# Optimization experiments

Hardware: AMD Instinct MI355X
Metric: run time of the kernel (lower is better)

The kernel has to match this reference:

```python
import jax, jax.numpy as jnp
import numpy as np

VOCAB, D, H = 100000, 128, 256
B, T = 64, 512


def setup_inputs() -> dict:
    key = jax.random.key(0)
    ks = jax.random.split(key, 7)
    path = jax.random.randint(ks[0], (B, T), 0, VOCAB, dtype=jnp.int32)
    valid_len = jax.random.randint(ks[1], (B,), 1, T + 1, dtype=jnp.int32)
    embedding = jax.random.normal(ks[2], (VOCAB, D), dtype=jnp.float32)
    s_ih = 1.0 / np.sqrt(H)
    W_ih = jax.random.uniform(ks[3], (4 * H, D), jnp.float32, -s_ih, s_ih)
    W_hh = jax.random.uniform(ks[4], (4 * H, H), jnp.float32, -s_ih, s_ih)
    b_ih = jax.random.uniform(ks[5], (4 * H,), jnp.float32, -s_ih, s_ih)
    b_hh = jax.random.uniform(ks[6], (4 * H,), jnp.float32, -s_ih, s_ih)
    return {"path": path, "valid_len": valid_len, "embedding": embedding,
            "W_ih": W_ih, "W_hh": W_hh, "b_ih": b_ih, "b_hh": b_hh}


def _lstm_last(x, valid_len, W_ih, W_hh, b_ih, b_hh):
    # x: [B, T, D] -> last-valid hidden state [B, H]
    Bx, Tx, _ = x.shape
    Hd = W_hh.shape[1]
    # precompute input projections for all steps: [T, B, 4H]
    xp = jnp.einsum('btd,gd->tbg', x, W_ih) + b_ih + b_hh

    def step(carry, xg):
        h, c = carry
        gates = xg + h @ W_hh.T  # [B, 4H]
        i, f, g, o = jnp.split(gates, 4, axis=-1)  # pytorch gate order i,f,g,o
        c = jax.nn.sigmoid(f) * c + jax.nn.sigmoid(i) * jnp.tanh(g)
        h = jax.nn.sigmoid(o) * jnp.tanh(c)
        return (h, c), h

    h0 = jnp.zeros((Bx, Hd), x.dtype)
    c0 = jnp.zeros((Bx, Hd), x.dtype)
    _, hs = jax.lax.scan(step, (h0, c0), xp)  # hs: [T, B, H]
    # gather output at t = valid_len - 1 (packed LSTM never advances past valid_len)
    return hs[valid_len - 1, jnp.arange(Bx)]


def reference(path, valid_len, embedding, W_ih, W_hh, b_ih, b_hh):
    x = embedding[path]  # [B, T, D] irregular gather
    return _lstm_last(x, valid_len, W_ih, W_hh, b_ih, b_hh)
```

## Files before the change

kernel.cpp:

```cpp
#include <hip/hip_runtime.h>
#include <stdint.h>


#define BB 64
#define TT 512
#define DD 128
#define HH 256

typedef __fp16 half2v __attribute__((ext_vector_type(2)));

__device__ __forceinline__ uint32_t pk_f16(float lo, float hi) {
    half2v h = __builtin_amdgcn_cvt_pkrtz(lo, hi);
    return __builtin_bit_cast(uint32_t, h);
}

__device__ __forceinline__ float dot2(uint32_t a, uint32_t b, float acc) {
#if __has_builtin(__builtin_amdgcn_fdot2)
    return __builtin_amdgcn_fdot2(__builtin_bit_cast(half2v, a),
                                  __builtin_bit_cast(half2v, b), acc, false);
#else
    half2v av = __builtin_bit_cast(half2v, a);
    half2v bv = __builtin_bit_cast(half2v, b);
    acc += (float)av[0] * (float)bv[0];
    acc += (float)av[1] * (float)bv[1];
    return acc;
#endif
}

__device__ __forceinline__ float fsig(float x)  { return 1.f / (1.f + __expf(-x)); }
__device__ __forceinline__ float ftanh(float x) { return 1.f - 2.f / (__expf(2.f * x) + 1.f); }

__global__ __launch_bounds__(1024, 4)
void lstm_cluster_kernel(const int* __restrict__ path, const int* __restrict__ vlen,
                         const float* __restrict__ emb, const float* __restrict__ Wih,
                         const float* __restrict__ Whh, const float* __restrict__ bih,
                         const float* __restrict__ bhh, float* __restrict__ out,
                         float* hslot ) {
    const int b   = blockIdx.x & (BB - 1);
    const int k   = blockIdx.x >> 6;
    const int tid = threadIdx.x;
    const int r   = tid >> 2;
    const int q   = tid & 3;
    const int g   = r >> 6;
    const int u   = r & 63;
    const int grow = (g << 8) + (k << 6) + u;

    __shared__ uint32_t h_pk[4][40];
    __shared__ uint32_t x_pk[2][4][24];
    __shared__ float    G[256];
    __shared__ int      path_l[TT];

    uint32_t whh[32];
    {
        const float* wr = Whh + grow * HH + (q << 6);
#pragma unroll
        for (int c = 0; c < 32; ++c) whh[c] = pk_f16(wr[2 * c], wr[2 * c + 1]);
    }
    uint32_t wih[16];
    {
        const float* wr = Wih + grow * DD + (q << 5);
#pragma unroll
        for (int c = 0; c < 16; ++c) wih[c] = pk_f16(wr[2 * c], wr[2 * c + 1]);
    }
    const float bias = bih[grow] + bhh[grow];
    const int   L    = vlen[b];

    if (tid < TT)  path_l[tid] = path[b * TT + tid];
    if (tid < 160) ((uint32_t*)h_pk)[tid] = 0u;
    __syncthreads();

    float xr_next = 0.f;
    if (tid < DD) {
        float x0 = emb[(size_t)path_l[0] * DD + tid];
        float hi = __shfl_xor(x0, 1);
        if (!(tid & 1)) x_pk[0][tid >> 5][(tid & 31) >> 1] = pk_f16(x0, hi);
        xr_next = emb[(size_t)path_l[L > 1 ? 1 : 0] * DD + tid];
    }
    float c_state = 0.f;
    __syncthreads();

    for (int t = 0; t < L; ++t) {
        const int slot  = t & 1;
        const int phase = (t >> 1) & 1;

        float xr_pf = 0.f;
        if (tid < DD) {
            int tpf = (t + 2 < TT) ? t + 2 : TT - 1;
            xr_pf = emb[(size_t)path_l[tpf] * DD + tid];
        }

        float acc = 0.f;
#pragma unroll
        for (int c = 0; c < 8; ++c) {
            uint4 hv = *(const uint4*)&h_pk[q][c << 2];
            acc = dot2(whh[(c << 2) + 0], hv.x, acc);
            acc = dot2(whh[(c << 2) + 1], hv.y, acc);
            acc = dot2(whh[(c << 2) + 2], hv.z, acc);
            acc = dot2(whh[(c << 2) + 3], hv.w, acc);
        }
#pragma unroll
        for (int c = 0; c < 4; ++c) {
            uint4 xv = *(const uint4*)&x_pk[slot][q][c << 2];
            acc = dot2(wih[(c << 2) + 0], xv.x, acc);
            acc = dot2(wih[(c << 2) + 1], xv.y, acc);
            acc = dot2(wih[(c << 2) + 2], xv.z, acc);
            acc = dot2(wih[(c << 2) + 3], xv.w, acc);
        }

        acc += __shfl_xor(acc, 1);
        acc += __shfl_xor(acc, 2);
        if (q == 0) G[r] = acc + bias;
        __syncthreads();

        if (tid < DD) {
            float hi = __shfl_xor(xr_next, 1);
            if (!(tid & 1)) x_pk[slot ^ 1][tid >> 5][(tid & 31) >> 1] = pk_f16(xr_next, hi);
        }
        if (tid < 64) {
            float gi = fsig(G[tid]);
            float gf = fsig(G[64 + tid]);
            float gg = ftanh(G[128 + tid]);
            float go = fsig(G[192 + tid]);
            c_state  = gf * c_state + gi * gg;
            float h  = go * ftanh(c_state);
            if (t == L - 1) out[b * HH + (k << 6) + tid] = h;
            __hip_atomic_store(&hslot[(slot * BB + b) * HH + (k << 6) + tid],
                               phase ? h + 8.f : h,
                               __ATOMIC_RELAXED, __HIP_MEMORY_SCOPE_AGENT);
        }
        xr_next = xr_pf;

        if (t < L - 1) {
            if (tid < HH) {
                float* addr = &hslot[(slot * BB + b) * HH + tid];
                float v;
                int spins = 0;
                if (phase == 0) {
                    do { v = __hip_atomic_load(addr, __ATOMIC_RELAXED, __HIP_MEMORY_SCOPE_AGENT);
                    } while (!(v > -4.f && v < 4.f) && ++spins < 200000);
                } else {
                    do { v = __hip_atomic_load(addr, __ATOMIC_RELAXED, __HIP_MEMORY_SCOPE_AGENT);
                    } while (!(v > 4.f) && ++spins < 200000);
                    v -= 8.f;
                }
                float hi = __shfl_xor(v, 1);
                if (!(tid & 1)) h_pk[tid >> 6][(tid & 63) >> 1] = pk_f16(v, hi);
            }
        }
        __syncthreads();
    }
}

extern "C" void kernel_launch(void* const* d_in, const int* in_sizes, int n_in,
                              void* d_out, int out_size, void* d_ws, size_t ws_size,
                              hipStream_t stream) {
    const int*   path = (const int*)d_in[0];
    const int*   vlen = (const int*)d_in[1];
    const float* emb  = (const float*)d_in[2];
    const float* Wih  = (const float*)d_in[3];
    const float* Whh  = (const float*)d_in[4];
    const float* bih  = (const float*)d_in[5];
    const float* bhh  = (const float*)d_in[6];

    (void)hipMemsetAsync(d_ws, 0x41, (size_t)2 * BB * HH * sizeof(float), stream);
    lstm_cluster_kernel<<<256, 1024, 0, stream>>>(path, vlen, emb, Wih, Whh, bih, bhh,
                                                  (float*)d_out, (float*)d_ws);
}
```

Measured before the change: 765.7 us.

## Exchange packed fp16 hidden state with bit-flip phase flags across blocks

The cross-block hidden-state exchange now sends fp16-packed pairs instead of fp32 values, halving the polled data. Phase is encoded by bitwise inversion, with readiness checked on exponent bits. Each block writes its own slice directly into shared memory and only polls the three remote slices, using separate waves (tids 896-991) so that polling runs in parallel with the gate wave and the embedding-prefetch wave. This aims to cut synchronization latency on the serial recurrence, but it relies on the fp16 bit-pattern check (|h|<2 keeps bit 14 clear) being a valid readiness flag.

```diff
diff --git a/kernel.cpp b/kernel.cpp
--- a/kernel.cpp
+++ b/kernel.cpp
@@ -35,7 +35,7 @@
                          const float* __restrict__ emb, const float* __restrict__ Wih,
                          const float* __restrict__ Whh, const float* __restrict__ bih,
                          const float* __restrict__ bhh, float* __restrict__ out,
-                         float* hslot ) {
+                         uint32_t* hx ) {
     const int b   = blockIdx.x & (BB - 1);
     const int k   = blockIdx.x >> 6;
     const int tid = threadIdx.x;
@@ -70,11 +70,12 @@
     __syncthreads();
 
     float xr_next = 0.f;
-    if (tid < DD) {
-        float x0 = emb[(size_t)path_l[0] * DD + tid];
+    if (tid >= 128 && tid < 256) {
+        int e = tid - 128;
+        float x0 = emb[(size_t)path_l[0] * DD + e];
         float hi = __shfl_xor(x0, 1);
-        if (!(tid & 1)) x_pk[0][tid >> 5][(tid & 31) >> 1] = pk_f16(x0, hi);
-        xr_next = emb[(size_t)path_l[L > 1 ? 1 : 0] * DD + tid];
+        if (!(e & 1)) x_pk[0][e >> 5][(e & 31) >> 1] = pk_f16(x0, hi);
+        xr_next = emb[(size_t)path_l[L > 1 ? 1 : 0] * DD + e];
     }
     float c_state = 0.f;
     __syncthreads();
@@ -82,12 +83,7 @@
     for (int t = 0; t < L; ++t) {
         const int slot  = t & 1;
         const int phase = (t >> 1) & 1;
-
-        float xr_pf = 0.f;
-        if (tid < DD) {
-            int tpf = (t + 2 < TT) ? t + 2 : TT - 1;
-            xr_pf = emb[(size_t)path_l[tpf] * DD + tid];
-        }
+        const uint32_t want = phase ? 0x40004000u : 0u;
 
         float acc = 0.f;
 #pragma unroll
@@ -106,16 +102,11 @@
             acc = dot2(wih[(c << 2) + 2], xv.z, acc);
             acc = dot2(wih[(c << 2) + 3], xv.w, acc);
         }
-
         acc += __shfl_xor(acc, 1);
         acc += __shfl_xor(acc, 2);
         if (q == 0) G[r] = acc + bias;
         __syncthreads();
 
-        if (tid < DD) {
-            float hi = __shfl_xor(xr_next, 1);
-            if (!(tid & 1)) x_pk[slot ^ 1][tid >> 5][(tid & 31) >> 1] = pk_f16(xr_next, hi);
-        }
         if (tid < 64) {
             float gi = fsig(G[tid]);
             float gf = fsig(G[64 + tid]);
@@ -124,28 +115,30 @@
             c_state  = gf * c_state + gi * gg;
             float h  = go * ftanh(c_state);
             if (t == L - 1) out[b * HH + (k << 6) + tid] = h;
-            __hip_atomic_store(&hslot[(slot * BB + b) * HH + (k << 6) + tid],
-                               phase ? h + 8.f : h,
-                               __ATOMIC_RELAXED, __HIP_MEMORY_SCOPE_AGENT);
-        }
-        xr_next = xr_pf;
-
-        if (t < L - 1) {
-            if (tid < HH) {
-                float* addr = &hslot[(slot * BB + b) * HH + tid];
-                float v;
-                int spins = 0;
-                if (phase == 0) {
-                    do { v = __hip_atomic_load(addr, __ATOMIC_RELAXED, __HIP_MEMORY_SCOPE_AGENT);
-                    } while (!(v > -4.f && v < 4.f) && ++spins < 200000);
-                } else {
-                    do { v = __hip_atomic_load(addr, __ATOMIC_RELAXED, __HIP_MEMORY_SCOPE_AGENT);
-                    } while (!(v > 4.f) && ++spins < 200000);
-                    v -= 8.f;
-                }
-                float hi = __shfl_xor(v, 1);
-                if (!(tid & 1)) h_pk[tid >> 6][(tid & 63) >> 1] = pk_f16(v, hi);
+            float h1 = __shfl_xor(h, 1);
+            if (!(tid & 1)) {
+                uint32_t pk = pk_f16(h, h1);
+                h_pk[k][tid >> 1] = pk;
+                __hip_atomic_store(&hx[(slot * BB + b) * 128 + (k << 5) + (tid >> 1)],
+                                   phase ? ~pk : pk,
+                                   __ATOMIC_RELAXED, __HIP_MEMORY_SCOPE_AGENT);
             }
+        } else if (tid >= 128 && tid < 256) {
+            int e = tid - 128;
+            float hi = __shfl_xor(xr_next, 1);
+            if (!(e & 1)) x_pk[slot ^ 1][e >> 5][(e & 31) >> 1] = pk_f16(xr_next, hi);
+            int tpf = (t + 2 < TT) ? t + 2 : TT - 1;
+            xr_next = emb[(size_t)path_l[tpf] * DD + e];
+        } else if (tid >= 896 && tid < 992 && t < L - 1) {
+            int j  = tid - 896;
+            int qq = j >> 5; if (qq >= k) ++qq;
+            int c  = j & 31;
+            uint32_t* addr = &hx[(slot * BB + b) * 128 + (qq << 5) + c];
+            uint32_t v; int spins = 0;
+            do {
+                v = __hip_atomic_load(addr, __ATOMIC_RELAXED, __HIP_MEMORY_SCOPE_AGENT);
+            } while ((v & 0x40004000u) != want && ++spins < (1 << 20));
+            h_pk[qq][c] = phase ? ~v : v;
         }
         __syncthreads();
     }
@@ -162,7 +155,7 @@
     const float* bih  = (const float*)d_in[5];
     const float* bhh  = (const float*)d_in[6];
 
-    (void)hipMemsetAsync(d_ws, 0x41, (size_t)2 * BB * HH * sizeof(float), stream);
+    (void)hipMemsetAsync(d_ws, 0xFF, (size_t)2 * BB * 128 * sizeof(uint32_t), stream);
     lstm_cluster_kernel<<<256, 1024, 0, stream>>>(path, vlen, emb, Wih, Whh, bih, bhh,
-                                                  (float*)d_out, (float*)d_ws);
+                                                  (float*)d_out, (uint32_t*)d_ws);
 }
```

Measured after the change: 679.5 us. -11.3%, faster.
